# Optimization experiments

Measured on AMD Instinct MI355X. Metric: run time of the kernel, lower is better.

Reference implementation:

```python
import jax, jax.numpy as jnp
import numpy as np

LN_EPS = 1e-5

def _mha(xq, xkv, in_w, in_b, out_w, out_b, n_heads):
    # torch nn.MultiheadAttention, batch_first=True, dropout=0
    B, S, d = xq.shape
    T = xkv.shape[1]
    dh = d // n_heads
    wq, wk, wv = jnp.split(in_w, 3, axis=0)   # each [d, d]
    bq, bk, bv = jnp.split(in_b, 3)
    q = (xq @ wq.T + bq).reshape(B, S, n_heads, dh).transpose(0, 2, 1, 3)
    k = (xkv @ wk.T + bk).reshape(B, T, n_heads, dh).transpose(0, 2, 1, 3)
    v = (xkv @ wv.T + bv).reshape(B, T, n_heads, dh).transpose(0, 2, 1, 3)
    scores = jnp.einsum('bhsd,bhtd->bhst', q, k) / jnp.sqrt(jnp.asarray(dh, xq.dtype))
    attn = jax.nn.softmax(scores, axis=-1)    # explicit [B,H,S,T] weights (need_weights=True path)
    o = jnp.einsum('bhst,bhtd->bhsd', attn, v)
    o = o.transpose(0, 2, 1, 3).reshape(B, S, d)
    return o @ out_w.T + out_b

def _ln(x, g, b):
    mu = jnp.mean(x, axis=-1, keepdims=True)
    var = jnp.mean(jnp.square(x - mu), axis=-1, keepdims=True)
    return (x - mu) / jnp.sqrt(var + LN_EPS) * g + b

def setup_inputs() -> dict:
    key = jax.random.key(0)
    B, S, T, d, ff = 4, 1024, 1024, 1024, 4096
    ks = jax.random.split(key, 10)
    s = 0.02
    return {
        'x': jax.random.normal(ks[0], (B, S, d), jnp.float32),
        'mem': jax.random.normal(ks[1], (B, T, d), jnp.float32),
        'sa_in_w': jax.random.normal(ks[2], (3 * d, d), jnp.float32) * s,
        'sa_in_b': jnp.zeros((3 * d,), jnp.float32),
        'sa_out_w': jax.random.normal(ks[3], (d, d), jnp.float32) * s,
        'sa_out_b': jnp.zeros((d,), jnp.float32),
        'ca_in_w': jax.random.normal(ks[4], (3 * d, d), jnp.float32) * s,
        'ca_in_b': jnp.zeros((3 * d,), jnp.float32),
        'ca_out_w': jax.random.normal(ks[5], (d, d), jnp.float32) * s,
        'ca_out_b': jnp.zeros((d,), jnp.float32),
        'ff_w1': jax.random.normal(ks[6], (ff, d), jnp.float32) * s,
        'ff_b1': jnp.zeros((ff,), jnp.float32),
        'ff_w2': jax.random.normal(ks[7], (d, ff), jnp.float32) * s,
        'ff_b2': jnp.zeros((d,), jnp.float32),
        'ln1_g': jnp.ones((d,), jnp.float32), 'ln1_b': jnp.zeros((d,), jnp.float32),
        'ln2_g': jnp.ones((d,), jnp.float32), 'ln2_b': jnp.zeros((d,), jnp.float32),
        'ln3_g': jnp.ones((d,), jnp.float32), 'ln3_b': jnp.zeros((d,), jnp.float32),
        'n_heads': 16,
    }

def reference(x, mem, sa_in_w, sa_in_b, sa_out_w, sa_out_b,
              ca_in_w, ca_in_b, ca_out_w, ca_out_b,
              ff_w1, ff_b1, ff_w2, ff_b2,
              ln1_g, ln1_b, ln2_g, ln2_b, ln3_g, ln3_b, n_heads):
    sa = _mha(x, x, sa_in_w, sa_in_b, sa_out_w, sa_out_b, n_heads)
    x = _ln(x + sa, ln1_g, ln1_b)
    ca = _mha(x, mem, ca_in_w, ca_in_b, ca_out_w, ca_out_b, n_heads)
    x = _ln(x + ca, ln2_g, ln2_b)
    h = jax.nn.gelu(x @ ff_w1.T + ff_b1, approximate=False)  # torch nn.GELU default = exact erf
    ff = h @ ff_w2.T + ff_b2
    return _ln(x + ff, ln3_g, ln3_b)
```

## Files before the change

### kernel.cpp

```cpp
#include <hip/hip_runtime.h>
#include <cstddef>

#define D_MODEL 1024
#define SEQ     1024
#define BATCH   4
#define NHEAD   16
#define DH      64
#define FFDIM   4096
#define NTOK    (BATCH*SEQ)

typedef float f32x4  __attribute__((ext_vector_type(4)));
typedef short bf16x8 __attribute__((ext_vector_type(8)));

static __device__ __forceinline__ unsigned short f2bf(float x){
  union { float f; unsigned u; } v; v.f = x;
  unsigned r = v.u + 0x7fffu + ((v.u >> 16) & 1u);
  return (unsigned short)(r >> 16);
}

static __device__ __forceinline__ float bf2f(unsigned short h){
  union { unsigned u; float f; } v; v.u = ((unsigned)h) << 16; return v.f;
}

static __device__ __forceinline__ void gl_lds16(const void* g, void* l){
  __builtin_amdgcn_global_load_lds((const __attribute__((address_space(1))) void*)g,
                                   (__attribute__((address_space(3))) void*)l, 16, 0, 0);
}

static __device__ __forceinline__ int2 swz_tile(int gx, int RX, int RY){
  int id = blockIdx.y * gx + blockIdx.x;
  int x = id & 7, s = id >> 3;
  int nrx = gx / RX;
  int bx = (x % nrx) * RX + (s % RX);
  int by = (x / nrx) * RY + (s / RX);
  return make_int2(bx, by);
}

struct CvtJobs {
  const float* src[8];
  unsigned short* dst[8];
  int n[8];
};

__global__ __launch_bounds__(256) void cvt_kernel(CvtJobs jobs){
  int seg = blockIdx.y;
  const float* s = jobs.src[seg];
  unsigned short* d = jobs.dst[seg];
  int n = jobs.n[seg];
  int stride = gridDim.x * 256 * 4;
  for (int i = (blockIdx.x*256 + threadIdx.x)*4; i < n; i += stride){
    float4 v = *(const float4*)(s + i);
    ushort4 o;
    o.x = f2bf(v.x); o.y = f2bf(v.y); o.z = f2bf(v.z); o.w = f2bf(v.w);
    *(ushort4*)(d + i) = o;
  }
}

template<int EPI>
static __device__ __forceinline__ void gemm_core(
    unsigned short* smem,
    const unsigned short* __restrict__ A,
    const unsigned short* __restrict__ B,
    const float* __restrict__ bias,
    void* __restrict__ out0,
    unsigned short* __restrict__ vt,
    int N, int K, int kbeg, int kend, int row0, int col0,
    int split, int ldout)
{
  unsigned short* As = smem;
  unsigned short* Bs = smem + 128*64;
  const int tid  = threadIdx.x;
  const int w    = tid >> 6, lane = tid & 63;
  const int quad = lane >> 4, l15 = lane & 15;
  const int lr   = lane >> 3, lc = lane & 7;
  const int csrc = lc ^ lr;
  const int sw   = l15 & 7;
  const int wm = (w >> 1) * 64, wn = (w & 1) * 64;

  f32x4 acc[4][4];
  const f32x4 zero4 = {0.f, 0.f, 0.f, 0.f};
  #pragma unroll
  for (int i=0;i<4;i++)
    #pragma unroll
    for (int j=0;j<4;j++)
      acc[i][j] = zero4;

  const unsigned short* Ag = A + (size_t)(row0 + lr)*K + csrc*8;
  const unsigned short* Bg = B + (size_t)(col0 + lr)*K + csrc*8;

  for (int k0 = kbeg; k0 < kend; k0 += 64){
    #pragma unroll
    for (int i=0;i<4;i++){
      gl_lds16(Ag + (size_t)(i*32 + w*8)*K + k0, &As[i*2048 + w*512]);
      gl_lds16(Bg + (size_t)(i*32 + w*8)*K + k0, &Bs[i*2048 + w*512]);
    }
    __syncthreads();
    #pragma unroll
    for (int ks=0; ks<2; ks++){
      bf16x8 af[4], bfr[4];
      #pragma unroll
      for (int i=0;i<4;i++)
        af[i] = *(const bf16x8*)&As[(wm + i*16 + l15)*64 + ((ks*4 + quad) ^ sw)*8];
      #pragma unroll
      for (int j=0;j<4;j++)
        bfr[j] = *(const bf16x8*)&Bs[(wn + j*16 + l15)*64 + ((ks*4 + quad) ^ sw)*8];
      #pragma unroll
      for (int i=0;i<4;i++)
        #pragma unroll
        for (int j=0;j<4;j++)
          acc[i][j] = __builtin_amdgcn_mfma_f32_16x16x32_bf16(af[i], bfr[j], acc[i][j], 0, 0, 0);
    }
    __syncthreads();
  }

  float bj[4];
  #pragma unroll
  for (int j=0;j<4;j++) bj[j] = bias[col0 + wn + j*16 + l15];

  #pragma unroll
  for (int i=0;i<4;i++){
    #pragma unroll
    for (int r=0;r<4;r++){
      int row = row0 + wm + i*16 + quad*4 + r;
      #pragma unroll
      for (int j=0;j<4;j++){
        int col = col0 + wn + j*16 + l15;
        float v = acc[i][j][r] + bj[j];
        if (EPI == 2){
          float t = 0.7978845608f * (v + 0.044715f * v * v * v);
          float e = __expf(2.f * t);
          float th = 1.f - 2.f * __builtin_amdgcn_rcpf(e + 1.f);
          v = 0.5f * v * (1.f + th);
        }
        if (EPI == 0){
          ((float*)out0)[(size_t)row*N + col] = v;
        } else if (EPI == 1 || EPI == 2){
          ((unsigned short*)out0)[(size_t)row*N + col] = f2bf(v);
        } else {
          if (col < split) ((unsigned short*)out0)[(size_t)row*ldout + col] = f2bf(v);
          else {
            int h = (col - split) >> 6, d = col & 63;
            int b = row >> 10, t = row & 1023;
            vt[((size_t)(b*NHEAD + h)*DH + d)*SEQ + t] = f2bf(v);
          }
        }
      }
    }
  }
}

template<int EPI>
__global__ __launch_bounds__(256) void gemm_swz(
    const unsigned short* A, const unsigned short* B, const float* bias,
    void* out0, unsigned short* vt, int N, int K, int split, int ldout,
    int RX, int RY)
{
  __shared__ __align__(16) unsigned short smem[2*128*64];
  int2 t = swz_tile(gridDim.x, RX, RY);
  gemm_core<EPI>(smem, A, B, bias, out0, vt, N, K, 0, K,
                 t.y*128, t.x*128, split, ldout);
}

__global__ __launch_bounds__(256) void gemm_split(
    const unsigned short* A, const unsigned short* B, const float* bias,
    unsigned short* outA, unsigned short* outB, int N, int K)
{
  __shared__ __align__(16) unsigned short smem[2*128*64];
  int2 t = swz_tile(gridDim.x, 4, 8);
  int kseg = K >> 1;
  int kbeg = blockIdx.z * kseg;
  unsigned short* o = blockIdx.z ? outB : outA;
  gemm_core<1>(smem, A, B, bias, o, nullptr, N, K, kbeg, kbeg + kseg,
               t.y*128, t.x*128, 0, 0);
}

__global__ __launch_bounds__(256) void gemm_ca(
    const unsigned short* x1b, const unsigned short* memb,
    const unsigned short* w, const float* biasq, const float* biaskv,
    unsigned short* qout, unsigned short* kout, unsigned short* vt)
{
  __shared__ __align__(16) unsigned short smem[2*128*64];
  int2 t = swz_tile(gridDim.x, 12, 8);
  const bool qs = t.x < 8;
  const unsigned short* A = qs ? x1b : memb;
  const unsigned short* B = qs ? w : w + (size_t)1024*1024;
  const float* bias       = qs ? biasq : biaskv;
  unsigned short* out     = qs ? qout : kout;
  const int col0          = qs ? t.x*128 : (t.x - 8)*128;
  gemm_core<5>(smem, A, B, bias, out, vt, 2048, 1024, 0, 1024,
               t.y*128, col0, 1024, 1024);
}

__global__ __launch_bounds__(256) void attn_kernel(
    const unsigned short* __restrict__ Q, int ldq,
    const unsigned short* __restrict__ Kp, int ldk,
    const unsigned short* __restrict__ Vt,
    unsigned short* __restrict__ O)
{
  __shared__ __align__(16) unsigned short Qs[128*64];
  __shared__ __align__(16) unsigned short Ks[64*64];
  __shared__ __align__(16) unsigned short Vs[64*64];
  __shared__ __align__(16) unsigned short Ps[4*32*72];

  const int tid  = threadIdx.x;
  const int w    = tid >> 6, lane = tid & 63;
  const int quad = lane >> 4, l15 = lane & 15;
  const int lr   = lane >> 3, lc = lane & 7;
  const int csrc = lc ^ lr;
  const int sw   = l15 & 7;
  const int id = blockIdx.x;
  const int xc = id & 7, s = id >> 3;
  const int bh = xc*8 + (s >> 3), qt = s & 7;
  const int b = bh >> 4, h = bh & 15;
  const int q0   = qt * 128;
  const int tok0 = b * SEQ;
  const int hoff = h * DH;

  #pragma unroll
  for (int i=0;i<4;i++){
    int r = i*32 + w*8 + lr;
    gl_lds16(Q + (size_t)(tok0 + q0 + r)*ldq + hoff + csrc*8, &Qs[i*2048 + w*512]);
  }
  __syncthreads();

  bf16x8 qb[2][2];
  #pragma unroll
  for (int qi=0;qi<2;qi++){
    int row = w*32 + qi*16 + l15;
    qb[qi][0] = *(const bf16x8*)&Qs[row*64 + ((0 + quad) ^ sw)*8];
    qb[qi][1] = *(const bf16x8*)&Qs[row*64 + ((4 + quad) ^ sw)*8];
  }

  float lsum[2] = {0.f, 0.f};
  f32x4 oacc[2][4];
  const f32x4 zero4 = {0.f, 0.f, 0.f, 0.f};
  #pragma unroll
  for (int qi=0;qi<2;qi++)
    #pragma unroll
    for (int dt=0;dt<4;dt++)
      oacc[qi][dt] = zero4;

  unsigned short* pw = &Ps[w*32*72];

  for (int kc = 0; kc < SEQ/64; ++kc){
    __syncthreads();
    #pragma unroll
    for (int i=0;i<2;i++){
      int r = i*32 + w*8 + lr;
      gl_lds16(Kp + (size_t)(tok0 + kc*64 + r)*ldk + hoff + csrc*8, &Ks[i*2048 + w*512]);
      gl_lds16(Vt + ((size_t)bh*DH + r)*SEQ + kc*64 + csrc*8,       &Vs[i*2048 + w*512]);
    }
    __syncthreads();

    #pragma unroll
    for (int tj=0;tj<4;tj++){
      bf16x8 ka0 = *(const bf16x8*)&Ks[(tj*16 + l15)*64 + ((0 + quad) ^ sw)*8];
      bf16x8 ka1 = *(const bf16x8*)&Ks[(tj*16 + l15)*64 + ((4 + quad) ^ sw)*8];
      #pragma unroll
      for (int qi=0;qi<2;qi++){
        f32x4 z = zero4;
        z = __builtin_amdgcn_mfma_f32_16x16x32_bf16(ka0, qb[qi][0], z, 0, 0, 0);
        z = __builtin_amdgcn_mfma_f32_16x16x32_bf16(ka1, qb[qi][1], z, 0, 0, 0);
        float p0 = __expf(z[0] * 0.125f);
        float p1 = __expf(z[1] * 0.125f);
        float p2 = __expf(z[2] * 0.125f);
        float p3 = __expf(z[3] * 0.125f);
        lsum[qi] += (p0 + p1) + (p2 + p3);
        short4 pk;
        pk.x = (short)f2bf(p0); pk.y = (short)f2bf(p1);
        pk.z = (short)f2bf(p2); pk.w = (short)f2bf(p3);
        *(short4*)&pw[(qi*16 + l15)*72 + tj*16 + quad*4] = pk;
      }
    }

    #pragma unroll
    for (int qi=0;qi<2;qi++){
      bf16x8 pa0 = *(const bf16x8*)&pw[(qi*16 + l15)*72 + quad*8];
      bf16x8 pa1 = *(const bf16x8*)&pw[(qi*16 + l15)*72 + 32 + quad*8];
      #pragma unroll
      for (int dt=0;dt<4;dt++){
        bf16x8 vb0 = *(const bf16x8*)&Vs[(dt*16 + l15)*64 + ((0 + quad) ^ sw)*8];
        bf16x8 vb1 = *(const bf16x8*)&Vs[(dt*16 + l15)*64 + ((4 + quad) ^ sw)*8];
        oacc[qi][dt] = __builtin_amdgcn_mfma_f32_16x16x32_bf16(pa0, vb0, oacc[qi][dt], 0, 0, 0);
        oacc[qi][dt] = __builtin_amdgcn_mfma_f32_16x16x32_bf16(pa1, vb1, oacc[qi][dt], 0, 0, 0);
      }
    }
  }

  #pragma unroll
  for (int qi=0;qi<2;qi++){
    lsum[qi] += __shfl_xor(lsum[qi], 16);
    lsum[qi] += __shfl_xor(lsum[qi], 32);
  }

  #pragma unroll
  for (int qi=0;qi<2;qi++){
    #pragma unroll
    for (int r=0;r<4;r++){
      float lv = __shfl(lsum[qi], quad*4 + r);
      float rinv = __builtin_amdgcn_rcpf(lv);
      size_t qrow = (size_t)(tok0 + q0 + w*32 + qi*16 + quad*4 + r);
      #pragma unroll
      for (int dt=0;dt<4;dt++)
        O[qrow*D_MODEL + hoff + dt*16 + l15] = f2bf(oacc[qi][dt][r] * rinv);
    }
  }
}

__global__ __launch_bounds__(256) void ln_kernel(
    const float* __restrict__ resid,
    const unsigned short* __restrict__ d1,
    const unsigned short* __restrict__ d2,
    const float* __restrict__ g, const float* __restrict__ beta,
    float* __restrict__ outf, unsigned short* __restrict__ outb)
{
  const int row = blockIdx.x;
  const int t = threadIdx.x;
  const size_t base = (size_t)row * D_MODEL;
  float4 a = *(const float4*)(resid + base + t*4);
  ushort4 p4 = *(const ushort4*)(d1 + base + t*4);
  ushort4 q4 = *(const ushort4*)(d2 + base + t*4);
  float v0 = a.x + bf2f(p4.x) + bf2f(q4.x);
  float v1 = a.y + bf2f(p4.y) + bf2f(q4.y);
  float v2 = a.z + bf2f(p4.z) + bf2f(q4.z);
  float v3 = a.w + bf2f(p4.w) + bf2f(q4.w);
  float s1 = v0+v1+v2+v3;
  float s2 = v0*v0+v1*v1+v2*v2+v3*v3;
  #pragma unroll
  for (int off=32; off>0; off>>=1){
    s1 += __shfl_down(s1, off);
    s2 += __shfl_down(s2, off);
  }
  __shared__ float red[8];
  const int wid = t >> 6;
  if ((t & 63) == 0){ red[wid*2] = s1; red[wid*2+1] = s2; }
  __syncthreads();
  s1 = red[0]+red[2]+red[4]+red[6];
  s2 = red[1]+red[3]+red[5]+red[7];
  float mean = s1 * (1.f/1024.f);
  float var  = s2 * (1.f/1024.f) - mean*mean;
  float rstd = rsqrtf(var + 1e-5f);
  float4 gg = *(const float4*)(g + t*4);
  float4 bb = *(const float4*)(beta + t*4);
  float y0 = (v0-mean)*rstd*gg.x + bb.x;
  float y1 = (v1-mean)*rstd*gg.y + bb.y;
  float y2 = (v2-mean)*rstd*gg.z + bb.z;
  float y3 = (v3-mean)*rstd*gg.w + bb.w;
  if (outf) *(float4*)(outf + base + t*4) = make_float4(y0,y1,y2,y3);
  if (outb){
    ushort4 o;
    o.x = f2bf(y0); o.y = f2bf(y1); o.z = f2bf(y2); o.w = f2bf(y3);
    *(ushort4*)(outb + base + t*4) = o;
  }
}

extern "C" void kernel_launch(void* const* d_in, const int* in_sizes, int n_in,
                              void* d_out, int out_size, void* d_ws, size_t ws_size,
                              hipStream_t stream)
{
  const float* x        = (const float*)d_in[0];
  const float* mem      = (const float*)d_in[1];
  const float* sa_in_w  = (const float*)d_in[2];
  const float* sa_in_b  = (const float*)d_in[3];
  const float* sa_out_w = (const float*)d_in[4];
  const float* sa_out_b = (const float*)d_in[5];
  const float* ca_in_w  = (const float*)d_in[6];
  const float* ca_in_b  = (const float*)d_in[7];
  const float* ca_out_w = (const float*)d_in[8];
  const float* ca_out_b = (const float*)d_in[9];
  const float* ff_w1    = (const float*)d_in[10];
  const float* ff_b1    = (const float*)d_in[11];
  const float* ff_w2    = (const float*)d_in[12];
  const float* ff_b2    = (const float*)d_in[13];
  const float* ln1_g    = (const float*)d_in[14];
  const float* ln1_b    = (const float*)d_in[15];
  const float* ln2_g    = (const float*)d_in[16];
  const float* ln2_b    = (const float*)d_in[17];
  const float* ln3_g    = (const float*)d_in[18];
  const float* ln3_b    = (const float*)d_in[19];

  char* base = (char*)d_ws;
  size_t off = 0;
  auto alloc = [&](size_t bytes) -> void* {
    void* r = base + off;
    off += (bytes + 255) & ~(size_t)255;
    return r;
  };
  unsigned short* xb     = (unsigned short*)alloc((size_t)NTOK*1024*2);
  unsigned short* memb   = (unsigned short*)alloc((size_t)NTOK*1024*2);
  unsigned short* wsain  = (unsigned short*)alloc((size_t)3072*1024*2);
  unsigned short* wsaout = (unsigned short*)alloc((size_t)1024*1024*2);
  unsigned short* wcain  = (unsigned short*)alloc((size_t)3072*1024*2);
  unsigned short* wcaout = (unsigned short*)alloc((size_t)1024*1024*2);
  unsigned short* wff1   = (unsigned short*)alloc((size_t)4096*1024*2);
  unsigned short* wff2   = (unsigned short*)alloc((size_t)4096*1024*2);
  unsigned short* qkvbuf = (unsigned short*)alloc((size_t)NTOK*3072*2);
  unsigned short* attnb  = (unsigned short*)alloc((size_t)NTOK*1024*2);
  float*          proj   = (float*)alloc((size_t)NTOK*1024*4);
  float*          x1f    = (float*)alloc((size_t)NTOK*1024*4);
  unsigned short* x1b    = (unsigned short*)alloc((size_t)NTOK*1024*2);
  float*          x2f    = (float*)alloc((size_t)NTOK*1024*4);
  unsigned short* x2b    = (unsigned short*)alloc((size_t)NTOK*1024*2);

  unsigned short* vt   = (unsigned short*)proj;
  unsigned short* hbuf = qkvbuf;
  unsigned short* pA   = (unsigned short*)proj;
  unsigned short* pB1  = (unsigned short*)x2f;
  unsigned short* pB2  = (unsigned short*)xb;
  unsigned short* pB3  = (unsigned short*)x1f;

  CvtJobs jobs;
  jobs.src[0]=x;        jobs.dst[0]=xb;     jobs.n[0]=NTOK*1024;
  jobs.src[1]=mem;      jobs.dst[1]=memb;   jobs.n[1]=NTOK*1024;
  jobs.src[2]=sa_in_w;  jobs.dst[2]=wsain;  jobs.n[2]=3072*1024;
  jobs.src[3]=sa_out_w; jobs.dst[3]=wsaout; jobs.n[3]=1024*1024;
  jobs.src[4]=ca_in_w;  jobs.dst[4]=wcain;  jobs.n[4]=3072*1024;
  jobs.src[5]=ca_out_w; jobs.dst[5]=wcaout; jobs.n[5]=1024*1024;
  jobs.src[6]=ff_w1;    jobs.dst[6]=wff1;   jobs.n[6]=4096*1024;
  jobs.src[7]=ff_w2;    jobs.dst[7]=wff2;   jobs.n[7]=4096*1024;
  cvt_kernel<<<dim3(1024,8), 256, 0, stream>>>(jobs);

  unsigned short* qk_sa = qkvbuf;
  gemm_swz<5><<<dim3(24,32), 256, 0, stream>>>(xb, wsain, sa_in_b, qk_sa, vt,
                                               3072, 1024, 2048, 2048, 12, 8);
  attn_kernel<<<512, 256, 0, stream>>>(qk_sa, 2048, qk_sa + 1024, 2048, vt, attnb);
  gemm_split<<<dim3(8,32,2), 256, 0, stream>>>(attnb, wsaout, sa_out_b, pA, pB1, 1024, 1024);
  ln_kernel<<<NTOK, 256, 0, stream>>>(x, pA, pB1, ln1_g, ln1_b, x1f, x1b);

  unsigned short* qca  = qkvbuf;
  unsigned short* kbuf = qkvbuf + (size_t)NTOK*1024;
  gemm_ca<<<dim3(24,32), 256, 0, stream>>>(x1b, memb, wcain, ca_in_b, ca_in_b + 1024,
                                           qca, kbuf, vt);
  attn_kernel<<<512, 256, 0, stream>>>(qca, 1024, kbuf, 1024, vt, attnb);
  gemm_split<<<dim3(8,32,2), 256, 0, stream>>>(attnb, wcaout, ca_out_b, pA, pB2, 1024, 1024);
  ln_kernel<<<NTOK, 256, 0, stream>>>(x1f, pA, pB2, ln2_g, ln2_b, x2f, x2b);

  gemm_swz<2><<<dim3(32,32), 256, 0, stream>>>(x2b, wff1, ff_b1, hbuf, nullptr,
                                               4096, 1024, 0, 0, 8, 16);
  gemm_split<<<dim3(8,32,2), 256, 0, stream>>>(hbuf, wff2, ff_b2, pA, pB3, 1024, 4096);
  ln_kernel<<<NTOK, 256, 0, stream>>>(x2f, pA, pB3, ln3_g, ln3_b, (float*)d_out, nullptr);
}
```

Baseline: 506.4 us.

## Fuse Q projection into attention, batch K/V projections, split FF2 four ways

The Q projection is computed inside the attention kernel, so Q never goes to global memory. The self- and cross-attention K/V projections become one 1024-block launch that can run up front, since neither depends on LN1. The FF2 GEMM is split along K into four partial bf16 outputs that the final layernorm sums, raising parallelism. The trade-offs are that each attention block now does a K=1024 GEMM before its main loop, which lengthens the kernel, and that four bf16 partial sums add rounding error and extra memory traffic in the layernorm.

```diff
diff --git a/kernel.cpp b/kernel.cpp
--- a/kernel.cpp
+++ b/kernel.cpp
@@ -132,9 +132,7 @@
           float th = 1.f - 2.f * __builtin_amdgcn_rcpf(e + 1.f);
           v = 0.5f * v * (1.f + th);
         }
-        if (EPI == 0){
-          ((float*)out0)[(size_t)row*N + col] = v;
-        } else if (EPI == 1 || EPI == 2){
+        if (EPI == 1 || EPI == 2){
           ((unsigned short*)out0)[(size_t)row*N + col] = f2bf(v);
         } else {
           if (col < split) ((unsigned short*)out0)[(size_t)row*ldout + col] = f2bf(v);
@@ -152,13 +150,31 @@
 template<int EPI>
 __global__ __launch_bounds__(256) void gemm_swz(
     const unsigned short* A, const unsigned short* B, const float* bias,
-    void* out0, unsigned short* vt, int N, int K, int split, int ldout,
-    int RX, int RY)
+    void* out0, int N, int K, int RX, int RY)
 {
   __shared__ __align__(16) unsigned short smem[2*128*64];
   int2 t = swz_tile(gridDim.x, RX, RY);
-  gemm_core<EPI>(smem, A, B, bias, out0, vt, N, K, 0, K,
-                 t.y*128, t.x*128, split, ldout);
+  gemm_core<EPI>(smem, A, B, bias, out0, nullptr, N, K, 0, K,
+                 t.y*128, t.x*128, 0, 0);
+}
+
+__global__ __launch_bounds__(256) void gemm_kv(
+    const unsigned short* xb, const unsigned short* memb,
+    const unsigned short* wsa, const unsigned short* wca,
+    const float* bsa, const float* bca,
+    unsigned short* ksa, unsigned short* vtsa,
+    unsigned short* kca, unsigned short* vtca)
+{
+  __shared__ __align__(16) unsigned short smem[2*128*64];
+  const int id = blockIdx.x;
+  const bool sa = id < 512;
+  const int hid = id & 511;
+  const int x = hid & 7, s = hid >> 3;
+  const int bx = (x & 1)*8 + (s & 7);
+  const int by = (x >> 1)*8 + (s >> 3);
+  gemm_core<5>(smem, sa ? xb : memb, sa ? wsa : wca, sa ? bsa : bca,
+               sa ? ksa : kca, sa ? vtsa : vtca,
+               2048, 1024, 0, 1024, by*128, bx*128, 1024, 1024);
 }
 
 __global__ __launch_bounds__(256) void gemm_split(
@@ -174,26 +190,26 @@
                t.y*128, t.x*128, 0, 0);
 }
 
-__global__ __launch_bounds__(256) void gemm_ca(
-    const unsigned short* x1b, const unsigned short* memb,
-    const unsigned short* w, const float* biasq, const float* biaskv,
-    unsigned short* qout, unsigned short* kout, unsigned short* vt)
+__global__ __launch_bounds__(256) void gemm_split4(
+    const unsigned short* A, const unsigned short* B, const float* bias,
+    unsigned short* o0, unsigned short* o1, unsigned short* o2, unsigned short* o3,
+    int N, int K)
 {
   __shared__ __align__(16) unsigned short smem[2*128*64];
-  int2 t = swz_tile(gridDim.x, 12, 8);
-  const bool qs = t.x < 8;
-  const unsigned short* A = qs ? x1b : memb;
-  const unsigned short* B = qs ? w : w + (size_t)1024*1024;
-  const float* bias       = qs ? biasq : biaskv;
-  unsigned short* out     = qs ? qout : kout;
-  const int col0          = qs ? t.x*128 : (t.x - 8)*128;
-  gemm_core<5>(smem, A, B, bias, out, vt, 2048, 1024, 0, 1024,
-               t.y*128, col0, 1024, 1024);
+  int2 t = swz_tile(gridDim.x, 4, 8);
+  int kseg = K >> 2;
+  int kbeg = blockIdx.z * kseg;
+  unsigned short* o = (blockIdx.z == 0) ? o0 : (blockIdx.z == 1) ? o1
+                    : (blockIdx.z == 2) ? o2 : o3;
+  gemm_core<1>(smem, A, B, bias, o, nullptr, N, K, kbeg, kbeg + kseg,
+               t.y*128, t.x*128, 0, 0);
 }
 
 __global__ __launch_bounds__(256) void attn_kernel(
-    const unsigned short* __restrict__ Q, int ldq,
-    const unsigned short* __restrict__ Kp, int ldk,
+    const unsigned short* __restrict__ Xa,
+    const unsigned short* __restrict__ Wq,
+    const float* __restrict__ bq,
+    const unsigned short* __restrict__ Kp,
     const unsigned short* __restrict__ Vt,
     unsigned short* __restrict__ O)
 {
@@ -216,10 +232,57 @@
   const int tok0 = b * SEQ;
   const int hoff = h * DH;
 
-  #pragma unroll
-  for (int i=0;i<4;i++){
-    int r = i*32 + w*8 + lr;
-    gl_lds16(Q + (size_t)(tok0 + q0 + r)*ldq + hoff + csrc*8, &Qs[i*2048 + w*512]);
+  f32x4 qacc[2][4];
+  const f32x4 zero4 = {0.f, 0.f, 0.f, 0.f};
+  #pragma unroll
+  for (int qi=0;qi<2;qi++)
+    #pragma unroll
+    for (int dj=0;dj<4;dj++)
+      qacc[qi][dj] = zero4;
+
+  const unsigned short* Ag = Xa + (size_t)(tok0 + q0 + lr)*1024 + csrc*8;
+  const unsigned short* Wg = Wq + (size_t)(hoff + lr)*1024 + csrc*8;
+
+  for (int k0 = 0; k0 < 1024; k0 += 64){
+    #pragma unroll
+    for (int i=0;i<4;i++)
+      gl_lds16(Ag + (size_t)(i*32 + w*8)*1024 + k0, &Qs[i*2048 + w*512]);
+    #pragma unroll
+    for (int i=0;i<2;i++)
+      gl_lds16(Wg + (size_t)(i*32 + w*8)*1024 + k0, &Ks[i*2048 + w*512]);
+    __syncthreads();
+    #pragma unroll
+    for (int ks=0; ks<2; ks++){
+      bf16x8 af[2], bfr[4];
+      #pragma unroll
+      for (int qi=0;qi<2;qi++)
+        af[qi] = *(const bf16x8*)&Qs[(w*32 + qi*16 + l15)*64 + ((ks*4 + quad) ^ sw)*8];
+      #pragma unroll
+      for (int dj=0;dj<4;dj++)
+        bfr[dj] = *(const bf16x8*)&Ks[(dj*16 + l15)*64 + ((ks*4 + quad) ^ sw)*8];
+      #pragma unroll
+      for (int qi=0;qi<2;qi++)
+        #pragma unroll
+        for (int dj=0;dj<4;dj++)
+          qacc[qi][dj] = __builtin_amdgcn_mfma_f32_16x16x32_bf16(af[qi], bfr[dj], qacc[qi][dj], 0, 0, 0);
+    }
+    __syncthreads();
+  }
+
+  {
+    float biasv[4];
+    #pragma unroll
+    for (int dj=0;dj<4;dj++) biasv[dj] = bq[hoff + dj*16 + l15];
+    #pragma unroll
+    for (int qi=0;qi<2;qi++)
+      #pragma unroll
+      for (int dj=0;dj<4;dj++)
+        #pragma unroll
+        for (int r=0;r<4;r++){
+          int q = w*32 + qi*16 + quad*4 + r;
+          int d = dj*16 + l15;
+          Qs[q*64 + (((d>>3) ^ (q&7))<<3) + (d&7)] = f2bf(qacc[qi][dj][r] + biasv[dj]);
+        }
   }
   __syncthreads();
 
@@ -233,7 +296,6 @@
 
   float lsum[2] = {0.f, 0.f};
   f32x4 oacc[2][4];
-  const f32x4 zero4 = {0.f, 0.f, 0.f, 0.f};
   #pragma unroll
   for (int qi=0;qi<2;qi++)
     #pragma unroll
@@ -247,8 +309,8 @@
     #pragma unroll
     for (int i=0;i<2;i++){
       int r = i*32 + w*8 + lr;
-      gl_lds16(Kp + (size_t)(tok0 + kc*64 + r)*ldk + hoff + csrc*8, &Ks[i*2048 + w*512]);
-      gl_lds16(Vt + ((size_t)bh*DH + r)*SEQ + kc*64 + csrc*8,       &Vs[i*2048 + w*512]);
+      gl_lds16(Kp + (size_t)(tok0 + kc*64 + r)*1024 + hoff + csrc*8, &Ks[i*2048 + w*512]);
+      gl_lds16(Vt + ((size_t)bh*DH + r)*SEQ + kc*64 + csrc*8,        &Vs[i*2048 + w*512]);
     }
     __syncthreads();
 
@@ -311,6 +373,8 @@
     const float* __restrict__ resid,
     const unsigned short* __restrict__ d1,
     const unsigned short* __restrict__ d2,
+    const unsigned short* __restrict__ d3,
+    const unsigned short* __restrict__ d4,
     const float* __restrict__ g, const float* __restrict__ beta,
     float* __restrict__ outf, unsigned short* __restrict__ outb)
 {
@@ -324,6 +388,14 @@
   float v1 = a.y + bf2f(p4.y) + bf2f(q4.y);
   float v2 = a.z + bf2f(p4.z) + bf2f(q4.z);
   float v3 = a.w + bf2f(p4.w) + bf2f(q4.w);
+  if (d3){
+    ushort4 r4 = *(const ushort4*)(d3 + base + t*4);
+    ushort4 s4 = *(const ushort4*)(d4 + base + t*4);
+    v0 += bf2f(r4.x) + bf2f(s4.x);
+    v1 += bf2f(r4.y) + bf2f(s4.y);
+    v2 += bf2f(r4.z) + bf2f(s4.z);
+    v3 += bf2f(r4.w) + bf2f(s4.w);
+  }
   float s1 = v0+v1+v2+v3;
   float s2 = v0*v0+v1*v1+v2*v2+v3*v3;
   #pragma unroll
@@ -402,12 +474,17 @@
   float*          x2f    = (float*)alloc((size_t)NTOK*1024*4);
   unsigned short* x2b    = (unsigned short*)alloc((size_t)NTOK*1024*2);
 
-  unsigned short* vt   = (unsigned short*)proj;
+  unsigned short* ksa  = qkvbuf;
+  unsigned short* vtsa = qkvbuf + (size_t)NTOK*1024;
+  unsigned short* kca  = qkvbuf + (size_t)NTOK*2048;
+  unsigned short* vtca = (unsigned short*)x2f;
   unsigned short* hbuf = qkvbuf;
   unsigned short* pA   = (unsigned short*)proj;
-  unsigned short* pB1  = (unsigned short*)x2f;
-  unsigned short* pB2  = (unsigned short*)xb;
-  unsigned short* pB3  = (unsigned short*)x1f;
+  unsigned short* pB   = (unsigned short*)xb;
+  unsigned short* q0p  = (unsigned short*)proj;
+  unsigned short* q1p  = (unsigned short*)proj + (size_t)NTOK*1024;
+  unsigned short* q2p  = (unsigned short*)x1f;
+  unsigned short* q3p  = (unsigned short*)x1f + (size_t)NTOK*1024;
 
   CvtJobs jobs;
   jobs.src[0]=x;        jobs.dst[0]=xb;     jobs.n[0]=NTOK*1024;
@@ -420,23 +497,20 @@
   jobs.src[7]=ff_w2;    jobs.dst[7]=wff2;   jobs.n[7]=4096*1024;
   cvt_kernel<<<dim3(1024,8), 256, 0, stream>>>(jobs);
 
-  unsigned short* qk_sa = qkvbuf;
-  gemm_swz<5><<<dim3(24,32), 256, 0, stream>>>(xb, wsain, sa_in_b, qk_sa, vt,
-                                               3072, 1024, 2048, 2048, 12, 8);
-  attn_kernel<<<512, 256, 0, stream>>>(qk_sa, 2048, qk_sa + 1024, 2048, vt, attnb);
-  gemm_split<<<dim3(8,32,2), 256, 0, stream>>>(attnb, wsaout, sa_out_b, pA, pB1, 1024, 1024);
-  ln_kernel<<<NTOK, 256, 0, stream>>>(x, pA, pB1, ln1_g, ln1_b, x1f, x1b);
-
-  unsigned short* qca  = qkvbuf;
-  unsigned short* kbuf = qkvbuf + (size_t)NTOK*1024;
-  gemm_ca<<<dim3(24,32), 256, 0, stream>>>(x1b, memb, wcain, ca_in_b, ca_in_b + 1024,
-                                           qca, kbuf, vt);
-  attn_kernel<<<512, 256, 0, stream>>>(qca, 1024, kbuf, 1024, vt, attnb);
-  gemm_split<<<dim3(8,32,2), 256, 0, stream>>>(attnb, wcaout, ca_out_b, pA, pB2, 1024, 1024);
-  ln_kernel<<<NTOK, 256, 0, stream>>>(x1f, pA, pB2, ln2_g, ln2_b, x2f, x2b);
-
-  gemm_swz<2><<<dim3(32,32), 256, 0, stream>>>(x2b, wff1, ff_b1, hbuf, nullptr,
-                                               4096, 1024, 0, 0, 8, 16);
-  gemm_split<<<dim3(8,32,2), 256, 0, stream>>>(hbuf, wff2, ff_b2, pA, pB3, 1024, 4096);
-  ln_kernel<<<NTOK, 256, 0, stream>>>(x2f, pA, pB3, ln3_g, ln3_b, (float*)d_out, nullptr);
-}
+  gemm_kv<<<1024, 256, 0, stream>>>(xb, memb,
+                                    wsain + (size_t)1024*1024, wcain + (size_t)1024*1024,
+                                    sa_in_b + 1024, ca_in_b + 1024,
+                                    ksa, vtsa, kca, vtca);
+
+  attn_kernel<<<512, 256, 0, stream>>>(xb, wsain, sa_in_b, ksa, vtsa, attnb);
+  gemm_split<<<dim3(8,32,2), 256, 0, stream>>>(attnb, wsaout, sa_out_b, pA, pB, 1024, 1024);
+  ln_kernel<<<NTOK, 256, 0, stream>>>(x, pA, pB, nullptr, nullptr, ln1_g, ln1_b, x1f, x1b);
+
+  attn_kernel<<<512, 256, 0, stream>>>(x1b, wcain, ca_in_b, kca, vtca, attnb);
+  gemm_split<<<dim3(8,32,2), 256, 0, stream>>>(attnb, wcaout, ca_out_b, pA, pB, 1024, 1024);
+  ln_kernel<<<NTOK, 256, 0, stream>>>(x1f, pA, pB, nullptr, nullptr, ln2_g, ln2_b, x2f, x2b);
+
+  gemm_swz<2><<<dim3(32,32), 256, 0, stream>>>(x2b, wff1, ff_b1, hbuf, 4096, 1024, 8, 16);
+  gemm_split4<<<dim3(8,32,4), 256, 0, stream>>>(hbuf, wff2, ff_b2, q0p, q1p, q2p, q3p, 1024, 4096);
+  ln_kernel<<<NTOK, 256, 0, stream>>>(x2f, q0p, q1p, q2p, q3p, ln3_g, ln3_b, (float*)d_out, nullptr);
+}
```

Measured after the change: 477.7 us. 1.06x faster.
